# Kernel optimization log

Hardware: AMD Instinct MI355X
Metric: run time of the kernel (lower is better)

Reference implementation:

```python
import math
import jax, jax.numpy as jnp
from jax import lax
import numpy as np

TWO_PI = 2.0 * math.pi
CG_ITERS = 30      # DifferentiableLinearSolver(max_iter=30)
CG_TOL = 1e-6
CG_REG = 1e-6      # reg = 1e-6 * I added inside the solver


def build_second_diff_matrix(N, dtype):
    e = jnp.ones(N, dtype)
    e2 = -2.0 * e
    e2 = e2.at[0].set(-1.0).at[-1].set(-1.0)
    oper = jnp.diag(e2) + jnp.diag(e[:-1], -1) + jnp.diag(e[:-1], 1)
    return oper.T @ oper


def cumtrapz(y, dx):
    # cumulative trapezoid along last axis, keeping length (leading zero)
    avg = (y[..., :-1] + y[..., 1:]) * (0.5 * dx)
    c = jnp.cumsum(avg, axis=-1)
    return jnp.concatenate([jnp.zeros_like(y[..., :1]), c], axis=-1)


def differ5(y, delta):
    mid = (y[..., 2:] - y[..., :-2]) / (2.0 * delta)
    first = (y[..., 1:2] - y[..., 0:1]) / delta
    last = (y[..., -1:] - y[..., -2:-1]) / delta
    return jnp.concatenate([first, mid, last], axis=-1)


def projec5(vec, var):
    # per-row norm-ball projection; vec: (B, N)
    M = vec.shape[-1]
    e = jnp.sqrt(M * var)
    n = jnp.linalg.norm(vec, axis=-1, keepdims=True)
    scale = jnp.where(n > e, e / jnp.maximum(n, 1e-30), 1.0)
    return vec * scale


def cg_solve(opedoub, coef, diagv, rhs, x0):
    # Solves (coef*opedoub + diag(diagv) + CG_REG*I) x = rhs via CG,
    # matching torch semantics (early break freezes state).
    def mv(p):
        return coef * (opedoub @ p) + (diagv + CG_REG) * p

    r0 = rhs - mv(x0)
    rs0 = jnp.dot(r0, r0)

    def step(carry, _):
        x, r, p, rsold, done = carry
        Ap = mv(p)
        a = rsold / (jnp.dot(p, Ap) + 1e-12)
        x1 = jnp.where(done, x, x + a * p)
        r1 = jnp.where(done, r, r - a * Ap)
        rsnew = jnp.dot(r1, r1)
        done1 = done | (jnp.sqrt(rsnew) < CG_TOL)
        bta = rsnew / (rsold + 1e-12)
        p1 = jnp.where(done1, p, r1 + bta * p)
        rsold1 = jnp.where(done1, rsold, rsnew)
        return (x1, r1, p1, rsold1, done1), None

    (x, _, _, _, _), _ = lax.scan(step, (x0, r0, r0, rs0, jnp.array(False)), None, length=CG_ITERS)
    return x


def _forward(s, eIF, xm, ym, sum_x, sum_y, lamuda, init_freqs, mode_mask,
             alpha, beta, var, fs, iteration,
             fe_w1, fe_b1, fe_w2, fe_b2,
             pr_w1, pr_b1, pr_w2, pr_b2, pr_w3, pr_b3, iter_weight):
    dtype = s.dtype
    B, N = s.shape
    K = eIF.shape[1]

    # ---- hyperparameter refinement MLP ----
    avg = jnp.mean(init_freqs, axis=1, keepdims=True)              # (B,1)
    h = jax.nn.relu(avg @ fe_w1.T + fe_b1)
    h = jax.nn.relu(h @ fe_w2.T + fe_b2)                            # (B,16)
    cur = jnp.stack([jnp.broadcast_to(alpha, (B,)),
                     jnp.broadcast_to(beta, (B,))], axis=1)         # (B,2)
    z = jnp.concatenate([h, cur], axis=1)                           # (B,18)
    z = jax.nn.relu(z @ pr_w1.T + pr_b1)
    z = jax.nn.relu(z @ pr_w2.T + pr_b2)
    res = jnp.tanh(z @ pr_w3.T + pr_b3)                             # (B,2)
    fac = jax.nn.sigmoid(iter_weight * iteration)
    res = res * fac * 0.1
    new_alpha = jnp.clip(alpha + jnp.mean(res[:, 0] * alpha), 1e-6, 0.01)
    new_beta = jnp.clip(beta + jnp.mean(res[:, 1] * beta), 1e-6, 0.1)

    betathr = jnp.minimum(10.0 ** (iteration / 36.0 - 10.0), new_beta)
    opedoub = build_second_diff_matrix(N, dtype)
    dx = 1.0 / fs

    # Within the torch k-loop, temp sums / lamuda / new_eIF[b,k] all still hold
    # their *input* values, so all (b,k) sub-problems are independent -> vmap.
    u = projec5(s - sum_x - sum_y - lamuda / new_alpha, var)        # (B,N)

    phase = TWO_PI * cumtrapz(eIF, dx)                               # (B,K,N)
    cosm = jnp.cos(phase)
    sinm = jnp.sin(phase)
    resid = (s[:, None, :] - (sum_x[:, None, :] - xm * cosm)
             - (sum_y[:, None, :] - ym * sinm)
             - u[:, None, :] - (lamuda / new_alpha)[:, None, :])
    rhs_x = cosm * resid
    rhs_y = sinm * resid

    coefA = 2.0 / new_alpha
    flat = lambda t: t.reshape(B * K, N)
    cg_v = jax.vmap(cg_solve, in_axes=(None, None, 0, 0, 0))

    xs = cg_v(opedoub, coefA, flat(cosm ** 2), flat(rhs_x), flat(xm)).reshape(B, K, N)
    ys = cg_v(opedoub, coefA, flat(sinm ** 2), flat(rhs_y), flat(ym)).reshape(B, K, N)

    xbar = differ5(xs, dx)
    ybar = differ5(ys, dx)
    denom = xs ** 2 + ys ** 2 + 1e-12
    deltaIF = (xs * ybar - ys * xbar) / (denom * TWO_PI)

    coefS = 2.0 / betathr
    ones_d = jnp.ones((B * K, N), dtype)
    zeros_d = jnp.zeros((B * K, N), dtype)
    smooth = cg_v(opedoub, coefS, ones_d, flat(deltaIF), zeros_d).reshape(B, K, N)
    eIF_s = eIF - 0.5 * smooth

    active = (mode_mask != 0)[:, :, None]                            # (B,K,1)
    new_xm = jnp.where(active, xs, xm)
    new_ym = jnp.where(active, ys, ym)
    new_eIF = jnp.where(active, eIF_s, eIF)

    new_phase = TWO_PI * cumtrapz(new_eIF, dx)
    maskf = active.astype(dtype)
    bsx = jnp.sum(maskf * new_xm * jnp.cos(new_phase), axis=1)       # (B,N)
    bsy = jnp.sum(maskf * new_ym * jnp.sin(new_phase), axis=1)
    new_lamuda = lamuda + new_alpha * (u + bsx + bsy - s)

    return (new_eIF, new_xm, new_ym, bsx, bsy, new_lamuda, new_alpha, new_beta)


def setup_inputs() -> dict:
    key = jax.random.key(0)
    B, K, N = 8, 4, 2048
    ks = jax.random.split(key, 20)
    f32 = jnp.float32
    inp = {
        "s": jax.random.normal(ks[0], (B, N), f32),
        "eIF": 50.0 + 200.0 * jax.random.uniform(ks[1], (B, K, N), f32),
        "xm": 0.1 * jax.random.normal(ks[2], (B, K, N), f32),
        "ym": 0.1 * jax.random.normal(ks[3], (B, K, N), f32),
        "sum_x": 0.1 * jax.random.normal(ks[4], (B, N), f32),
        "sum_y": 0.1 * jax.random.normal(ks[5], (B, N), f32),
        "lamuda": 0.01 * jax.random.normal(ks[6], (B, N), f32),
        "init_freqs": 50.0 + 200.0 * jax.random.uniform(ks[7], (B, K), f32),
        "mode_mask": jnp.ones((B, K), jnp.int32),
        "alpha": jnp.asarray(0.005, f32),
        "beta": jnp.asarray(0.05, f32),
        "var": jnp.asarray(0.01, f32),
        "fs": jnp.asarray(2000.0, f32),
        "iteration": 1,
        # HyperparameterRefinement params (torch Linear: y = x @ W.T + b)
        "fe_w1": 0.1 * jax.random.normal(ks[8], (32, 1), f32),
        "fe_b1": jnp.zeros((32,), f32),
        "fe_w2": 0.1 * jax.random.normal(ks[9], (16, 32), f32),
        "fe_b2": jnp.zeros((16,), f32),
        "pr_w1": 0.1 * jax.random.normal(ks[10], (64, 18), f32),
        "pr_b1": jnp.zeros((64,), f32),
        "pr_w2": 0.1 * jax.random.normal(ks[11], (32, 64), f32),
        "pr_b2": jnp.zeros((32,), f32),
        "pr_w3": 0.1 * jax.random.normal(ks[12], (2, 32), f32),
        "pr_b3": jnp.zeros((2,), f32),
        "iter_weight": jnp.asarray(0.1, f32),
    }
    return inp


def reference(s, eIF, xm, ym, sum_x, sum_y, lamuda, init_freqs, mode_mask,
              alpha, beta, var, fs, iteration,
              fe_w1, fe_b1, fe_w2, fe_b2,
              pr_w1, pr_b1, pr_w2, pr_b2, pr_w3, pr_b3, iter_weight):
    return _forward(s, eIF, xm, ym, sum_x, sum_y, lamuda, init_freqs, mode_mask,
                    alpha, beta, var, fs, iteration,
                    fe_w1, fe_b1, fe_w2, fe_b2,
                    pr_w1, pr_b1, pr_w2, pr_b2, pr_w3, pr_b3, iter_weight)
```

## Files before the change

### kernel.cpp

```cpp
#include <hip/hip_runtime.h>
#include <math.h>

#define Nq 2048
#define Bq 8
#define Kq 4
#define BKq 32
#define NL 32
#define TWO_PI_D 6.283185307179586
#define PI_D 3.141592653589793
#define INV2PI_D 0.15915494309189535


__device__ __forceinline__ double wave_sum_d(double v) {
#pragma unroll
  for (int off = 1; off < 64; off <<= 1) v += __shfl_xor(v, off, 64);
  return v;
}

__device__ __forceinline__ float dpp_sum_f32(float v) {
  v += __int_as_float(__builtin_amdgcn_update_dpp(0, __float_as_int(v), 0x111, 0xf, 0xf, false));
  v += __int_as_float(__builtin_amdgcn_update_dpp(0, __float_as_int(v), 0x112, 0xf, 0xf, false));
  v += __int_as_float(__builtin_amdgcn_update_dpp(0, __float_as_int(v), 0x114, 0xf, 0xe, false));
  v += __int_as_float(__builtin_amdgcn_update_dpp(0, __float_as_int(v), 0x118, 0xf, 0xc, false));
  v += __int_as_float(__builtin_amdgcn_update_dpp(0, __float_as_int(v), 0x142, 0xa, 0xf, false));
  v += __int_as_float(__builtin_amdgcn_update_dpp(0, __float_as_int(v), 0x143, 0xc, 0xf, false));
  return __int_as_float(__builtin_amdgcn_readlane(__float_as_int(v), 63));
}

__device__ __forceinline__ float dpp_up1(float v) {
  return __int_as_float(__builtin_amdgcn_update_dpp(0, __float_as_int(v), 0x138, 0xf, 0xf, false));
}
__device__ __forceinline__ float dpp_dn1(float v) {
  return __int_as_float(__builtin_amdgcn_update_dpp(0, __float_as_int(v), 0x130, 0xf, 0xf, false));
}

__device__ __forceinline__ double lane_excl_prefix_d(double T, int lane) {
  double acc = T;
#pragma unroll
  for (int off = 1; off < 64; off <<= 1) {
    double t = __shfl_up(acc, off, 64);
    if (lane >= off) acc += t;
  }
  return acc - T;
}

__device__ __forceinline__ void fast_sincos_ph(double ph, float* sn, float* cs) {
  double k = trunc(ph * INV2PI_D);
  float phr = (float)(ph - k * TWO_PI_D);
  __sincosf(phr, sn, cs);
}

template <bool UNIT>
__device__ __forceinline__ void applyA(const float* p, float* Ap,
                                       const float* dd, float c, float c3,
                                       float c4, float ddu, int lane) {
  float lm1 = dpp_up1(p[NL - 1]);
  float lm2 = dpp_up1(p[NL - 2]);
  float rp1 = dpp_dn1(p[0]);
  float rp2 = dpp_dn1(p[1]);
#pragma unroll
  for (int e = 0; e < NL; ++e) {
    float m2 = (e >= 2) ? p[e - 2] : (e == 1 ? lm1 : lm2);
    float m1 = (e >= 1) ? p[e - 1] : lm1;
    float q1 = (e <= NL - 2) ? p[e + 1] : rp1;
    float q2 = (e <= NL - 3) ? p[e + 2] : (e == NL - 2 ? rp1 : rp2);
    float t1 = m2 + q2, t2 = m1 + q1;
    float u = fmaf(c, t1, -(c4 * t2));
    float d = UNIT ? ddu : dd[e];
    Ap[e] = fmaf(d, p[e], u);
  }
  if (lane == 0) {
    float d0 = (UNIT ? ddu : dd[0]) - c4;
    Ap[0] = fmaf(d0, p[0], fmaf(c, p[2], -(c3 * p[1])));
    float d1 = UNIT ? ddu : dd[1];
    Ap[1] = fmaf(d1, p[1], -(c3 * p[0])) + fmaf(c, p[3], -(c4 * p[2]));
  }
  if (lane == 63) {
    float dm2 = UNIT ? ddu : dd[NL - 2];
    Ap[NL - 2] = fmaf(dm2, p[NL - 2], c * p[NL - 4]) -
                 fmaf(c4, p[NL - 3], c3 * p[NL - 1]);
    float dm1 = (UNIT ? ddu : dd[NL - 1]) - c4;
    Ap[NL - 1] = fmaf(dm1, p[NL - 1], c * p[NL - 3]) - c3 * p[NL - 2];
  }
}

template <bool UNIT>
__device__ __forceinline__ void cg_wave_f(float coef, float* dd, float* r,
                                          float* x, int lane) {
  const float c = coef, c3 = 3.0f * coef, c4 = 4.0f * coef;
  const float ddu = 6.0f * coef + (1.0f + 1e-6f);
  if (!UNIT) {
#pragma unroll
    for (int e = 0; e < NL; ++e) dd[e] += 6.0f * coef;
  }
  float p[NL], Ap[NL];
  applyA<UNIT>(x, Ap, dd, c, c3, c4, ddu, lane);
  float s0 = 0, s1 = 0, s2 = 0, s3 = 0;
#pragma unroll
  for (int e = 0; e < NL; ++e) {
    r[e] -= Ap[e];
    p[e] = r[e];
    float* acc = (e & 2) ? ((e & 1) ? &s3 : &s2) : ((e & 1) ? &s1 : &s0);
    *acc = fmaf(r[e], r[e], *acc);
  }
  float rsold = dpp_sum_f32((s0 + s1) + (s2 + s3));
  for (int it = 0; it < 30; ++it) {
    applyA<UNIT>(p, Ap, dd, c, c3, c4, ddu, lane);
    float d0 = 0, d1 = 0, d2 = 0, d3 = 0;
#pragma unroll
    for (int e = 0; e < NL; ++e) {
      float* acc = (e & 2) ? ((e & 1) ? &d3 : &d2) : ((e & 1) ? &d1 : &d0);
      *acc = fmaf(p[e], Ap[e], *acc);
    }
    float pap = dpp_sum_f32((d0 + d1) + (d2 + d3));
    float a = __fdividef(rsold, pap + 1e-12f);
    float t0 = 0, t1 = 0, t2 = 0, t3 = 0;
#pragma unroll
    for (int e = 0; e < NL; ++e) {
      x[e] = fmaf(a, p[e], x[e]);
      r[e] = fmaf(-a, Ap[e], r[e]);
      float* acc = (e & 2) ? ((e & 1) ? &t3 : &t2) : ((e & 1) ? &t1 : &t0);
      *acc = fmaf(r[e], r[e], *acc);
    }
    float rsnew = dpp_sum_f32((t0 + t1) + (t2 + t3));
    if (rsnew < 1e-12f) break;
    float bta = __fdividef(rsnew, rsold + 1e-12f);
#pragma unroll
    for (int e = 0; e < NL; ++e) p[e] = fmaf(bta, p[e], r[e]);
    rsold = rsnew;
  }
}

__device__ __forceinline__ double blk_reduce(double v, double* sh) {
#pragma unroll
  for (int off = 32; off > 0; off >>= 1) v += __shfl_down(v, off, 64);
  int wid = threadIdx.x >> 6;
  int lane = threadIdx.x & 63;
  __syncthreads();
  if (lane == 0) sh[wid] = v;
  __syncthreads();
  double r = sh[0] + sh[1] + sh[2] + sh[3];
  __syncthreads();
  return r;
}

__global__ __launch_bounds__(128, 1) void row_kernel(
    const float* __restrict__ s, const float* __restrict__ eIF,
    const float* __restrict__ xm, const float* __restrict__ ym,
    const float* __restrict__ sum_x, const float* __restrict__ sum_y,
    const float* __restrict__ lamuda, const float* __restrict__ init_freqs,
    const int* __restrict__ mode_mask, const float* __restrict__ alpha_p,
    const float* __restrict__ beta_p, const float* __restrict__ var_p,
    const float* __restrict__ fs_p, const int* __restrict__ iter_p,
    const float* __restrict__ fe_w1, const float* __restrict__ fe_b1,
    const float* __restrict__ fe_w2, const float* __restrict__ fe_b2,
    const float* __restrict__ pr_w1, const float* __restrict__ pr_b1,
    const float* __restrict__ pr_w2, const float* __restrict__ pr_b2,
    const float* __restrict__ pr_w3, const float* __restrict__ pr_b3,
    const float* __restrict__ iter_w_p, double* __restrict__ hdr,
    float* __restrict__ out_eIF, float* __restrict__ out_xm,
    float* __restrict__ out_ym, float* __restrict__ cx_w,
    float* __restrict__ cy_w, float* __restrict__ out_scal) {
  __shared__ double sh_avg[Bq];
  __shared__ double sh_h1[Bq][32];
  __shared__ double sh_z[Bq][18];
  __shared__ double sh_z1[Bq][64];
  __shared__ double sh_z2[Bq][32];
  __shared__ double sh_res[Bq][2];
  __shared__ double sh_hdr[6];
  __shared__ float sh_xs[Nq], sh_ys[Nq];

  const int tid = threadIdx.x;
  const int wv = tid >> 6, lane = tid & 63;
  const int row = blockIdx.x, b = row >> 2;
  const int bb = b * Nq, base = row * Nq;

  double alpha = (double)alpha_p[0], beta = (double)beta_p[0];
  double iterv = (double)iter_p[0];
  if (tid < Bq) {
    double avg = 0.0;
#pragma unroll
    for (int k = 0; k < Kq; ++k) avg += (double)init_freqs[tid * Kq + k];
    sh_avg[tid] = avg * (1.0 / Kq);
  }
  __syncthreads();
  for (int n = tid; n < 256; n += 128) {
    int b2 = n >> 5, j = n & 31;
    double v = (double)fe_w1[j] * sh_avg[b2] + (double)fe_b1[j];
    sh_h1[b2][j] = v > 0.0 ? v : 0.0;
  }
  __syncthreads();
  {
    int b2 = tid >> 4, j = tid & 15;
    double acc = (double)fe_b2[j];
    for (int i = 0; i < 32; ++i) acc += (double)fe_w2[j * 32 + i] * sh_h1[b2][i];
    sh_z[b2][j] = acc > 0.0 ? acc : 0.0;
  }
  if (tid < Bq) {
    sh_z[tid][16] = alpha;
    sh_z[tid][17] = beta;
  }
  __syncthreads();
  for (int n = tid; n < 512; n += 128) {
    int b2 = n >> 6, j = n & 63;
    double acc = (double)pr_b1[j];
    for (int i = 0; i < 18; ++i) acc += (double)pr_w1[j * 18 + i] * sh_z[b2][i];
    sh_z1[b2][j] = acc > 0.0 ? acc : 0.0;
  }
  __syncthreads();
  for (int n = tid; n < 256; n += 128) {
    int b2 = n >> 5, j = n & 31;
    double acc = (double)pr_b2[j];
    for (int i = 0; i < 64; ++i) acc += (double)pr_w2[j * 64 + i] * sh_z1[b2][i];
    sh_z2[b2][j] = acc > 0.0 ? acc : 0.0;
  }
  __syncthreads();
  if (tid < 16) {
    int b2 = tid >> 1, c = tid & 1;
    double acc = (double)pr_b3[c];
    for (int i = 0; i < 32; ++i) acc += (double)pr_w3[c * 32 + i] * sh_z2[b2][i];
    double fac = 1.0 / (1.0 + exp(-(double)iter_w_p[0] * iterv));
    sh_res[b2][c] = tanh(acc) * fac * 0.1;
  }
  __syncthreads();
  if (tid == 0) {
    double r0 = 0.0, r1 = 0.0;
    for (int q = 0; q < Bq; ++q) { r0 += sh_res[q][0]; r1 += sh_res[q][1]; }
    double na = fmin(fmax(alpha + r0 * alpha * (1.0 / Bq), 1e-6), 0.01);
    double nb = fmin(fmax(beta + r1 * beta * (1.0 / Bq), 1e-6), 0.1);
    double betathr = fmin(pow(10.0, iterv / 36.0 - 10.0), nb);
    sh_hdr[0] = na;
    sh_hdr[1] = 2.0 / na;
    sh_hdr[2] = 2.0 / betathr;
    sh_hdr[3] = 1.0 / na;
    hdr[0] = na;
    hdr[4] = 1.0 / na;
    out_scal[0] = (float)na;
    out_scal[1] = (float)nb;
  }
  __syncthreads();
  const float coefA = (float)sh_hdr[1];
  const float coefS = (float)sh_hdr[2];
  const double inva = sh_hdr[3];

  double tv[NL];
  {
    double n0 = 0.0, n1 = 0.0;
#pragma unroll
    for (int e = 0; e < NL; ++e) {
      int gi = bb + lane * NL + e;
      tv[e] = (double)s[gi] - (double)sum_x[gi] - (double)sum_y[gi] -
              (double)lamuda[gi] * inva;
      ((e & 1) ? n1 : n0) += tv[e] * tv[e];
    }
    double nsq = wave_sum_d(n0 + n1);
    double nn = sqrt(nsq);
    double ee = sqrt((double)Nq * (double)var_p[0]);
    double scale = (nn > ee) ? ee / fmax(nn, 1e-30) : 1.0;
    double oms = 1.0 - scale;
#pragma unroll
    for (int e = 0; e < NL; ++e) tv[e] *= oms;
  }

  const double dx = 1.0 / (double)fs_p[0];
  const double c0 = PI_D * dx;
  float df[NL], r[NL], x[NL];
  {
    double ev[NL], pl[NL];
#pragma unroll
    for (int e = 0; e < NL; ++e) ev[e] = (double)eIF[base + lane * NL + e];
    pl[0] = ev[0];
#pragma unroll
    for (int e = 1; e < NL; ++e) pl[e] = pl[e - 1] + ev[e];
    double offs = lane_excl_prefix_d(pl[NL - 1], lane);
    double y0 = __shfl(ev[0], 0, 64);
#pragma unroll
    for (int e = 0; e < NL; ++e) {
      int i = lane * NL + e;
      double ph = c0 * (2.0 * (offs + pl[e]) - ev[e] - y0);
      float sn, cs;
      fast_sincos_ph(ph, &sn, &cs);
      float xmv = xm[base + i], ymv = ym[base + i];
      double resid = tv[e] + (double)xmv * (double)cs + (double)ymv * (double)sn;
      if (wv == 0) {
        df[e] = cs * cs + 1e-6f;
        r[e] = (float)((double)cs * resid);
        x[e] = xmv;
      } else {
        df[e] = sn * sn + 1e-6f;
        r[e] = (float)((double)sn * resid);
        x[e] = ymv;
      }
    }
  }

  cg_wave_f<false>(coefA, df, r, x, lane);

  {
    float* dst = (wv == 0) ? sh_xs : sh_ys;
#pragma unroll
    for (int e = 0; e < NL; ++e) dst[e * 64 + lane] = x[e];
  }
  __syncthreads();

  {
    float xs[NL], ys[NL];
#pragma unroll
    for (int e = 0; e < NL; ++e) {
      xs[e] = sh_xs[e * 64 + lane];
      ys[e] = sh_ys[e * 64 + lane];
    }
    float invdx = (float)fs_p[0], inv2dx = 0.5f * invdx;
    float xl = __shfl_up(xs[NL - 1], 1, 64), xr = __shfl_down(xs[0], 1, 64);
    float yl = __shfl_up(ys[NL - 1], 1, 64), yr = __shfl_down(ys[0], 1, 64);
#pragma unroll
    for (int e = 0; e < NL; ++e) {
      int i = lane * NL + e;
      float xm1 = (e >= 1) ? xs[e - 1] : xl;
      float xp1 = (e <= NL - 2) ? xs[e + 1] : xr;
      float ym1 = (e >= 1) ? ys[e - 1] : yl;
      float yp1 = (e <= NL - 2) ? ys[e + 1] : yr;
      float xb, yb;
      if (i == 0) {
        xb = (xp1 - xs[e]) * invdx;
        yb = (yp1 - ys[e]) * invdx;
      } else if (i == Nq - 1) {
        xb = (xs[e] - xm1) * invdx;
        yb = (ys[e] - ym1) * invdx;
      } else {
        xb = (xp1 - xm1) * inv2dx;
        yb = (yp1 - ym1) * inv2dx;
      }
      float denom = xs[e] * xs[e] + ys[e] * ys[e] + 1e-12f;
      r[e] = (xs[e] * yb - ys[e] * xb) / (denom * (float)TWO_PI_D);
      x[e] = 0.0f;
    }
  }

  cg_wave_f<true>(coefS, nullptr, r, x, lane);

  bool active = mode_mask[row] != 0;
  double eifn[NL], pl[NL];
#pragma unroll
  for (int e = 0; e < NL; ++e) {
    int i = base + lane * NL + e;
    double eifv = (double)eIF[i];
    eifn[e] = active ? (eifv - 0.5 * (double)x[e]) : eifv;
  }
  if (wv == 0) {
#pragma unroll
    for (int e = 0; e < NL; ++e) {
      int i = base + lane * NL + e;
      out_eIF[i] = (float)eifn[e];
      out_xm[i] = active ? sh_xs[e * 64 + lane] : xm[i];
    }
  } else {
#pragma unroll
    for (int e = 0; e < NL; ++e) {
      int i = base + lane * NL + e;
      out_ym[i] = active ? sh_ys[e * 64 + lane] : ym[i];
    }
  }
  pl[0] = eifn[0];
#pragma unroll
  for (int e = 1; e < NL; ++e) pl[e] = pl[e - 1] + eifn[e];
  double offs = lane_excl_prefix_d(pl[NL - 1], lane);
  double y0 = __shfl(eifn[0], 0, 64);
#pragma unroll
  for (int e = 0; e < NL; ++e) {
    int i = base + lane * NL + e;
    double ph = c0 * (2.0 * (offs + pl[e]) - eifn[e] - y0);
    float sn, cs;
    fast_sincos_ph(ph, &sn, &cs);
    if (wv == 0)
      cx_w[i] = active ? sh_xs[e * 64 + lane] * cs : 0.0f;
    else
      cy_w[i] = active ? sh_ys[e * 64 + lane] * sn : 0.0f;
  }
}

__global__ __launch_bounds__(256) void final_kernel(
    const float* __restrict__ s, const float* __restrict__ sum_x,
    const float* __restrict__ sum_y, const float* __restrict__ lamuda,
    const float* __restrict__ var_p, const double* __restrict__ hdr,
    const float* __restrict__ cx_w, const float* __restrict__ cy_w,
    float* __restrict__ out_bsx, float* __restrict__ out_bsy,
    float* __restrict__ out_lam) {
  __shared__ double sh_red[4];
  __shared__ double sh_scale;
  int b = blockIdx.x;
  int bb = b * Nq;
  int tid = threadIdx.x;
  double na = hdr[0], inva = hdr[4];
  double t[8];
  double loc = 0.0;
#pragma unroll
  for (int e = 0; e < 8; ++e) {
    int gi = bb + tid + e * 256;
    t[e] = (double)s[gi] - (double)sum_x[gi] - (double)sum_y[gi] -
           (double)lamuda[gi] * inva;
    loc += t[e] * t[e];
  }
  double nsq = blk_reduce(loc, sh_red);
  if (tid == 0) {
    double n = sqrt(nsq);
    double ee = sqrt((double)Nq * (double)var_p[0]);
    sh_scale = (n > ee) ? ee / fmax(n, 1e-30) : 1.0;
  }
  __syncthreads();
  double scale = sh_scale;
#pragma unroll
  for (int e = 0; e < 8; ++e) {
    int i = tid + e * 256;
    int gi = bb + i;
    double bx = 0.0, by = 0.0;
#pragma unroll
    for (int k = 0; k < Kq; ++k) {
      bx += (double)cx_w[(b * Kq + k) * Nq + i];
      by += (double)cy_w[(b * Kq + k) * Nq + i];
    }
    double u = t[e] * scale;
    double nl = (double)lamuda[gi] + na * (u + bx + by - (double)s[gi]);
    out_bsx[gi] = (float)bx;
    out_bsy[gi] = (float)by;
    out_lam[gi] = (float)nl;
  }
}

extern "C" void kernel_launch(void* const* d_in, const int* in_sizes, int n_in,
                              void* d_out, int out_size, void* d_ws, size_t ws_size,
                              hipStream_t stream) {
  (void)in_sizes; (void)n_in; (void)out_size; (void)ws_size;
  const float* s = (const float*)d_in[0];
  const float* eIF = (const float*)d_in[1];
  const float* xm = (const float*)d_in[2];
  const float* ym = (const float*)d_in[3];
  const float* sum_x = (const float*)d_in[4];
  const float* sum_y = (const float*)d_in[5];
  const float* lamuda = (const float*)d_in[6];
  const float* init_freqs = (const float*)d_in[7];
  const int* mode_mask = (const int*)d_in[8];
  const float* alpha = (const float*)d_in[9];
  const float* beta = (const float*)d_in[10];
  const float* var = (const float*)d_in[11];
  const float* fs = (const float*)d_in[12];
  const int* iteration = (const int*)d_in[13];
  const float* fe_w1 = (const float*)d_in[14];
  const float* fe_b1 = (const float*)d_in[15];
  const float* fe_w2 = (const float*)d_in[16];
  const float* fe_b2 = (const float*)d_in[17];
  const float* pr_w1 = (const float*)d_in[18];
  const float* pr_b1 = (const float*)d_in[19];
  const float* pr_w2 = (const float*)d_in[20];
  const float* pr_b2 = (const float*)d_in[21];
  const float* pr_w3 = (const float*)d_in[22];
  const float* pr_b3 = (const float*)d_in[23];
  const float* iter_weight = (const float*)d_in[24];

  float* out = (float*)d_out;
  const int BN = Bq * Nq;
  const int BKN = BKq * Nq;
  float* out_eIF = out;
  float* out_xm = out + BKN;
  float* out_ym = out + 2 * BKN;
  float* out_bsx = out + 3 * BKN;
  float* out_bsy = out + 3 * BKN + BN;
  float* out_lam = out + 3 * BKN + 2 * BN;
  float* out_scal = out + 3 * BKN + 3 * BN;

  double* W = (double*)d_ws;
  double* hdr = W;
  float* F = (float*)(W + 16);
  float* cx_w = F;
  float* cy_w = F + BKN;

  row_kernel<<<BKq, 128, 0, stream>>>(
      s, eIF, xm, ym, sum_x, sum_y, lamuda, init_freqs, mode_mask, alpha, beta,
      var, fs, iteration, fe_w1, fe_b1, fe_w2, fe_b2, pr_w1, pr_b1, pr_w2,
      pr_b2, pr_w3, pr_b3, iter_weight, hdr, out_eIF, out_xm, out_ym, cx_w,
      cy_w, out_scal);
  final_kernel<<<Bq, 256, 0, stream>>>(s, sum_x, sum_y, lamuda, var, hdr, cx_w,
                                       cy_w, out_bsx, out_bsy, out_lam);
}
```

Before: 172.3 us.

## Fuse row and final kernels into one per-batch kernel with shared-memory accumulation

Replaces the two-launch scheme (32 blocks of 128 threads, then 8 blocks of 256) with a single launch of 8 blocks of 512 threads, so each block handles all four modes of one batch. Per-mode sums of x*cos and y*sin are built with shared-memory atomics instead of being written to a global workspace and re-read. The lambda update reuses the projection scale already computed in the block. This removes a kernel launch and the global round trip, but uses 8 large blocks instead of 32 small ones and relies on LDS atomic adds, which may change float summation order.

```diff
diff --git a/kernel.cpp b/kernel.cpp
--- a/kernel.cpp
+++ b/kernel.cpp
@@ -4,7 +4,6 @@
 #define Nq 2048
 #define Bq 8
 #define Kq 4
-#define BKq 32
 #define NL 32
 #define TWO_PI_D 6.283185307179586
 #define PI_D 3.141592653589793
@@ -131,20 +130,7 @@
   }
 }
 
-__device__ __forceinline__ double blk_reduce(double v, double* sh) {
-#pragma unroll
-  for (int off = 32; off > 0; off >>= 1) v += __shfl_down(v, off, 64);
-  int wid = threadIdx.x >> 6;
-  int lane = threadIdx.x & 63;
-  __syncthreads();
-  if (lane == 0) sh[wid] = v;
-  __syncthreads();
-  double r = sh[0] + sh[1] + sh[2] + sh[3];
-  __syncthreads();
-  return r;
-}
-
-__global__ __launch_bounds__(128, 1) void row_kernel(
+__global__ __launch_bounds__(512, 2) void mega_kernel(
     const float* __restrict__ s, const float* __restrict__ eIF,
     const float* __restrict__ xm, const float* __restrict__ ym,
     const float* __restrict__ sum_x, const float* __restrict__ sum_y,
@@ -157,23 +143,32 @@
     const float* __restrict__ pr_w1, const float* __restrict__ pr_b1,
     const float* __restrict__ pr_w2, const float* __restrict__ pr_b2,
     const float* __restrict__ pr_w3, const float* __restrict__ pr_b3,
-    const float* __restrict__ iter_w_p, double* __restrict__ hdr,
-    float* __restrict__ out_eIF, float* __restrict__ out_xm,
-    float* __restrict__ out_ym, float* __restrict__ cx_w,
-    float* __restrict__ cy_w, float* __restrict__ out_scal) {
+    const float* __restrict__ iter_w_p, float* __restrict__ out_eIF,
+    float* __restrict__ out_xm, float* __restrict__ out_ym,
+    float* __restrict__ out_bsx, float* __restrict__ out_bsy,
+    float* __restrict__ out_lam, float* __restrict__ out_scal) {
   __shared__ double sh_avg[Bq];
   __shared__ double sh_h1[Bq][32];
-  __shared__ double sh_z[Bq][18];
+  __shared__ double sh_zz[Bq][18];
   __shared__ double sh_z1[Bq][64];
   __shared__ double sh_z2[Bq][32];
   __shared__ double sh_res[Bq][2];
-  __shared__ double sh_hdr[6];
-  __shared__ float sh_xs[Nq], sh_ys[Nq];
+  __shared__ double sh_hdr[4];
+  __shared__ double sh_scale_d;
+  __shared__ float sh_xs[Kq][Nq], sh_ys[Kq][Nq];
+  __shared__ float sh_bsx[Nq], sh_bsy[Nq];
 
   const int tid = threadIdx.x;
   const int wv = tid >> 6, lane = tid & 63;
-  const int row = blockIdx.x, b = row >> 2;
+  const int rr = wv >> 1, syst = wv & 1;
+  const int b = blockIdx.x;
+  const int row = b * Kq + rr;
   const int bb = b * Nq, base = row * Nq;
+
+  for (int j = tid; j < Nq; j += 512) {
+    sh_bsx[j] = 0.f;
+    sh_bsy[j] = 0.f;
+  }
 
   double alpha = (double)alpha_p[0], beta = (double)beta_p[0];
   double iterv = (double)iter_p[0];
@@ -184,32 +179,32 @@
     sh_avg[tid] = avg * (1.0 / Kq);
   }
   __syncthreads();
-  for (int n = tid; n < 256; n += 128) {
-    int b2 = n >> 5, j = n & 31;
+  if (tid < 256) {
+    int b2 = tid >> 5, j = tid & 31;
     double v = (double)fe_w1[j] * sh_avg[b2] + (double)fe_b1[j];
     sh_h1[b2][j] = v > 0.0 ? v : 0.0;
   }
   __syncthreads();
-  {
+  if (tid < 128) {
     int b2 = tid >> 4, j = tid & 15;
     double acc = (double)fe_b2[j];
     for (int i = 0; i < 32; ++i) acc += (double)fe_w2[j * 32 + i] * sh_h1[b2][i];
-    sh_z[b2][j] = acc > 0.0 ? acc : 0.0;
-  }
-  if (tid < Bq) {
-    sh_z[tid][16] = alpha;
-    sh_z[tid][17] = beta;
-  }
-  __syncthreads();
-  for (int n = tid; n < 512; n += 128) {
-    int b2 = n >> 6, j = n & 63;
+    sh_zz[b2][j] = acc > 0.0 ? acc : 0.0;
+  }
+  if (tid >= 128 && tid < 128 + Bq) {
+    sh_zz[tid - 128][16] = alpha;
+    sh_zz[tid - 128][17] = beta;
+  }
+  __syncthreads();
+  {
+    int b2 = tid >> 6, j = tid & 63;
     double acc = (double)pr_b1[j];
-    for (int i = 0; i < 18; ++i) acc += (double)pr_w1[j * 18 + i] * sh_z[b2][i];
+    for (int i = 0; i < 18; ++i) acc += (double)pr_w1[j * 18 + i] * sh_zz[b2][i];
     sh_z1[b2][j] = acc > 0.0 ? acc : 0.0;
   }
   __syncthreads();
-  for (int n = tid; n < 256; n += 128) {
-    int b2 = n >> 5, j = n & 31;
+  if (tid < 256) {
+    int b2 = tid >> 5, j = tid & 31;
     double acc = (double)pr_b2[j];
     for (int i = 0; i < 64; ++i) acc += (double)pr_w2[j * 64 + i] * sh_z1[b2][i];
     sh_z2[b2][j] = acc > 0.0 ? acc : 0.0;
@@ -227,16 +222,16 @@
     double r0 = 0.0, r1 = 0.0;
     for (int q = 0; q < Bq; ++q) { r0 += sh_res[q][0]; r1 += sh_res[q][1]; }
     double na = fmin(fmax(alpha + r0 * alpha * (1.0 / Bq), 1e-6), 0.01);
-    double nb = fmin(fmax(beta + r1 * beta * (1.0 / Bq), 1e-6), 0.1);
-    double betathr = fmin(pow(10.0, iterv / 36.0 - 10.0), nb);
+    double nb2 = fmin(fmax(beta + r1 * beta * (1.0 / Bq), 1e-6), 0.1);
+    double betathr = fmin(pow(10.0, iterv / 36.0 - 10.0), nb2);
     sh_hdr[0] = na;
     sh_hdr[1] = 2.0 / na;
     sh_hdr[2] = 2.0 / betathr;
     sh_hdr[3] = 1.0 / na;
-    hdr[0] = na;
-    hdr[4] = 1.0 / na;
-    out_scal[0] = (float)na;
-    out_scal[1] = (float)nb;
+    if (b == 0) {
+      out_scal[0] = (float)na;
+      out_scal[1] = (float)nb2;
+    }
   }
   __syncthreads();
   const float coefA = (float)sh_hdr[1];
@@ -257,6 +252,7 @@
     double nn = sqrt(nsq);
     double ee = sqrt((double)Nq * (double)var_p[0]);
     double scale = (nn > ee) ? ee / fmax(nn, 1e-30) : 1.0;
+    if (tid == 0) sh_scale_d = scale;
     double oms = 1.0 - scale;
 #pragma unroll
     for (int e = 0; e < NL; ++e) tv[e] *= oms;
@@ -264,7 +260,7 @@
 
   const double dx = 1.0 / (double)fs_p[0];
   const double c0 = PI_D * dx;
-  float df[NL], r[NL], x[NL];
+  float dd[NL], r[NL], x[NL];
   {
     double ev[NL], pl[NL];
 #pragma unroll
@@ -282,22 +278,22 @@
       fast_sincos_ph(ph, &sn, &cs);
       float xmv = xm[base + i], ymv = ym[base + i];
       double resid = tv[e] + (double)xmv * (double)cs + (double)ymv * (double)sn;
-      if (wv == 0) {
-        df[e] = cs * cs + 1e-6f;
+      if (syst == 0) {
+        dd[e] = cs * cs + 1e-6f;
         r[e] = (float)((double)cs * resid);
         x[e] = xmv;
       } else {
-        df[e] = sn * sn + 1e-6f;
+        dd[e] = sn * sn + 1e-6f;
         r[e] = (float)((double)sn * resid);
         x[e] = ymv;
       }
     }
   }
 
-  cg_wave_f<false>(coefA, df, r, x, lane);
-
-  {
-    float* dst = (wv == 0) ? sh_xs : sh_ys;
+  cg_wave_f<false>(coefA, dd, r, x, lane);
+
+  {
+    float* dst = (syst == 0) ? sh_xs[rr] : sh_ys[rr];
 #pragma unroll
     for (int e = 0; e < NL; ++e) dst[e * 64 + lane] = x[e];
   }
@@ -307,8 +303,8 @@
     float xs[NL], ys[NL];
 #pragma unroll
     for (int e = 0; e < NL; ++e) {
-      xs[e] = sh_xs[e * 64 + lane];
-      ys[e] = sh_ys[e * 64 + lane];
+      xs[e] = sh_xs[rr][e * 64 + lane];
+      ys[e] = sh_ys[rr][e * 64 + lane];
     }
     float invdx = (float)fs_p[0], inv2dx = 0.5f * invdx;
     float xl = __shfl_up(xs[NL - 1], 1, 64), xr = __shfl_down(xs[0], 1, 64);
@@ -347,18 +343,18 @@
     double eifv = (double)eIF[i];
     eifn[e] = active ? (eifv - 0.5 * (double)x[e]) : eifv;
   }
-  if (wv == 0) {
+  if (syst == 0) {
 #pragma unroll
     for (int e = 0; e < NL; ++e) {
       int i = base + lane * NL + e;
       out_eIF[i] = (float)eifn[e];
-      out_xm[i] = active ? sh_xs[e * 64 + lane] : xm[i];
+      out_xm[i] = active ? sh_xs[rr][e * 64 + lane] : xm[i];
     }
   } else {
 #pragma unroll
     for (int e = 0; e < NL; ++e) {
       int i = base + lane * NL + e;
-      out_ym[i] = active ? sh_ys[e * 64 + lane] : ym[i];
+      out_ym[i] = active ? sh_ys[rr][e * 64 + lane] : ym[i];
     }
   }
   pl[0] = eifn[0];
@@ -366,71 +362,44 @@
   for (int e = 1; e < NL; ++e) pl[e] = pl[e - 1] + eifn[e];
   double offs = lane_excl_prefix_d(pl[NL - 1], lane);
   double y0 = __shfl(eifn[0], 0, 64);
-#pragma unroll
-  for (int e = 0; e < NL; ++e) {
-    int i = base + lane * NL + e;
-    double ph = c0 * (2.0 * (offs + pl[e]) - eifn[e] - y0);
-    float sn, cs;
-    fast_sincos_ph(ph, &sn, &cs);
-    if (wv == 0)
-      cx_w[i] = active ? sh_xs[e * 64 + lane] * cs : 0.0f;
-    else
-      cy_w[i] = active ? sh_ys[e * 64 + lane] * sn : 0.0f;
-  }
-}
-
-__global__ __launch_bounds__(256) void final_kernel(
-    const float* __restrict__ s, const float* __restrict__ sum_x,
-    const float* __restrict__ sum_y, const float* __restrict__ lamuda,
-    const float* __restrict__ var_p, const double* __restrict__ hdr,
-    const float* __restrict__ cx_w, const float* __restrict__ cy_w,
-    float* __restrict__ out_bsx, float* __restrict__ out_bsy,
-    float* __restrict__ out_lam) {
-  __shared__ double sh_red[4];
-  __shared__ double sh_scale;
-  int b = blockIdx.x;
-  int bb = b * Nq;
-  int tid = threadIdx.x;
-  double na = hdr[0], inva = hdr[4];
-  double t[8];
-  double loc = 0.0;
-#pragma unroll
-  for (int e = 0; e < 8; ++e) {
-    int gi = bb + tid + e * 256;
-    t[e] = (double)s[gi] - (double)sum_x[gi] - (double)sum_y[gi] -
-           (double)lamuda[gi] * inva;
-    loc += t[e] * t[e];
-  }
-  double nsq = blk_reduce(loc, sh_red);
-  if (tid == 0) {
-    double n = sqrt(nsq);
-    double ee = sqrt((double)Nq * (double)var_p[0]);
-    sh_scale = (n > ee) ? ee / fmax(n, 1e-30) : 1.0;
-  }
-  __syncthreads();
-  double scale = sh_scale;
-#pragma unroll
-  for (int e = 0; e < 8; ++e) {
-    int i = tid + e * 256;
-    int gi = bb + i;
-    double bx = 0.0, by = 0.0;
-#pragma unroll
-    for (int k = 0; k < Kq; ++k) {
-      bx += (double)cx_w[(b * Kq + k) * Nq + i];
-      by += (double)cy_w[(b * Kq + k) * Nq + i];
-    }
-    double u = t[e] * scale;
-    double nl = (double)lamuda[gi] + na * (u + bx + by - (double)s[gi]);
-    out_bsx[gi] = (float)bx;
-    out_bsy[gi] = (float)by;
-    out_lam[gi] = (float)nl;
+  if (active) {
+#pragma unroll
+    for (int e = 0; e < NL; ++e) {
+      int i = lane * NL + e;
+      double ph = c0 * (2.0 * (offs + pl[e]) - eifn[e] - y0);
+      float sn, cs;
+      fast_sincos_ph(ph, &sn, &cs);
+      if (syst == 0)
+        atomicAdd(&sh_bsx[i], sh_xs[rr][e * 64 + lane] * cs);
+      else
+        atomicAdd(&sh_bsy[i], sh_ys[rr][e * 64 + lane] * sn);
+    }
+  }
+  __syncthreads();
+
+  {
+    double na = sh_hdr[0];
+    double scale = sh_scale_d;
+#pragma unroll
+    for (int j = 0; j < 4; ++j) {
+      int i = tid + j * 512;
+      int gi = bb + i;
+      double t = (double)s[gi] - (double)sum_x[gi] - (double)sum_y[gi] -
+                 (double)lamuda[gi] * inva;
+      double u = t * scale;
+      double bx = (double)sh_bsx[i], by = (double)sh_bsy[i];
+      double nl = (double)lamuda[gi] + na * (u + bx + by - (double)s[gi]);
+      out_bsx[gi] = (float)bx;
+      out_bsy[gi] = (float)by;
+      out_lam[gi] = (float)nl;
+    }
   }
 }
 
 extern "C" void kernel_launch(void* const* d_in, const int* in_sizes, int n_in,
                               void* d_out, int out_size, void* d_ws, size_t ws_size,
                               hipStream_t stream) {
-  (void)in_sizes; (void)n_in; (void)out_size; (void)ws_size;
+  (void)in_sizes; (void)n_in; (void)out_size; (void)d_ws; (void)ws_size;
   const float* s = (const float*)d_in[0];
   const float* eIF = (const float*)d_in[1];
   const float* xm = (const float*)d_in[2];
@@ -459,7 +428,7 @@
 
   float* out = (float*)d_out;
   const int BN = Bq * Nq;
-  const int BKN = BKq * Nq;
+  const int BKN = 4 * BN;
   float* out_eIF = out;
   float* out_xm = out + BKN;
   float* out_ym = out + 2 * BKN;
@@ -468,17 +437,9 @@
   float* out_lam = out + 3 * BKN + 2 * BN;
   float* out_scal = out + 3 * BKN + 3 * BN;
 
-  double* W = (double*)d_ws;
-  double* hdr = W;
-  float* F = (float*)(W + 16);
-  float* cx_w = F;
-  float* cy_w = F + BKN;
-
-  row_kernel<<<BKq, 128, 0, stream>>>(
+  mega_kernel<<<Bq, 512, 0, stream>>>(
       s, eIF, xm, ym, sum_x, sum_y, lamuda, init_freqs, mode_mask, alpha, beta,
       var, fs, iteration, fe_w1, fe_b1, fe_w2, fe_b2, pr_w1, pr_b1, pr_w2,
-      pr_b2, pr_w3, pr_b3, iter_weight, hdr, out_eIF, out_xm, out_ym, cx_w,
-      cy_w, out_scal);
-  final_kernel<<<Bq, 256, 0, stream>>>(s, sum_x, sum_y, lamuda, var, hdr, cx_w,
-                                       cy_w, out_bsx, out_bsy, out_lam);
-}
+      pr_b2, pr_w3, pr_b3, iter_weight, out_eIF, out_xm, out_ym, out_bsx,
+      out_bsy, out_lam, out_scal);
+}
```

Result: slower. 232.8 us (+35.1%).
